# Optimization experiments

Measured on AMD Instinct MI355X. Metric: run time of the kernel, lower is better.

## Reference

```python
import jax, jax.numpy as jnp
import numpy as np

NEG_SLOPE = 0.2  # PyG GATConv LeakyReLU slope


def _gat_conv(x, ei, W, a_src, a_dst, bias, concat):
    # x: [N, F_in], ei: [2, E] (with self-loops), W: [F_in, H*C], a_*: [H, C]
    N = x.shape[0]
    H, C = a_src.shape
    xp = (x @ W).reshape(N, H, C)                       # [N, H, C]
    src, dst = ei[0], ei[1]
    s_score = jnp.einsum('nhc,hc->nh', xp, a_src)       # [N, H]
    d_score = jnp.einsum('nhc,hc->nh', xp, a_dst)       # [N, H]
    e = jax.nn.leaky_relu(s_score[src] + d_score[dst], negative_slope=NEG_SLOPE)  # [E, H]
    # segment softmax over incoming edges of each dst node
    m = jax.ops.segment_max(e, dst, num_segments=N)     # [N, H]
    ex = jnp.exp(e - m[dst])                            # [E, H]
    den = jax.ops.segment_sum(ex, dst, num_segments=N)  # [N, H]
    alpha = ex / den[dst]                               # [E, H]
    msg = alpha[:, :, None] * xp[src]                   # [E, H, C]
    out = jax.ops.segment_sum(msg, dst, num_segments=N) # [N, H, C]
    out = out.reshape(N, H * C) if concat else out.mean(axis=1)
    return out + bias


def _add_self_loops(edge_index, num_nodes):
    ar = jnp.arange(num_nodes, dtype=edge_index.dtype)
    return jnp.concatenate([edge_index, jnp.stack([ar, ar])], axis=1)


def setup_inputs() -> dict:
    key = jax.random.key(0)
    ks = jax.random.split(key, 16)
    N, E, F_in, Hd, heads, out_c, G = 50000, 800000, 128, 64, 4, 10, 64
    x = jax.random.normal(ks[0], (N, F_in), dtype=jnp.float32)
    edge_index = jax.random.randint(ks[1], (2, E), 0, N, dtype=jnp.int64)
    batch = jnp.sort(jax.random.randint(ks[2], (N,), 0, G, dtype=jnp.int64))
    sc = lambda f: 1.0 / np.sqrt(f)
    # layer 1: in -> hidden, heads=4, concat
    W1 = jax.random.normal(ks[3], (F_in, heads * Hd), dtype=jnp.float32) * sc(F_in)
    a_src1 = jax.random.normal(ks[4], (heads, Hd), dtype=jnp.float32) * sc(Hd)
    a_dst1 = jax.random.normal(ks[5], (heads, Hd), dtype=jnp.float32) * sc(Hd)
    b1 = jnp.zeros((heads * Hd,), dtype=jnp.float32)
    # layer 2: heads*hidden -> hidden, heads=1, concat=False
    W2 = jax.random.normal(ks[6], (heads * Hd, Hd), dtype=jnp.float32) * sc(heads * Hd)
    a_src2 = jax.random.normal(ks[7], (1, Hd), dtype=jnp.float32) * sc(Hd)
    a_dst2 = jax.random.normal(ks[8], (1, Hd), dtype=jnp.float32) * sc(Hd)
    b2 = jnp.zeros((Hd,), dtype=jnp.float32)
    # final linear
    Wl = jax.random.normal(ks[9], (Hd, out_c), dtype=jnp.float32) * sc(Hd)
    bl = jnp.zeros((out_c,), dtype=jnp.float32)
    return {"x": x, "edge_index": edge_index, "batch": batch,
            "W1": W1, "a_src1": a_src1, "a_dst1": a_dst1, "b1": b1,
            "W2": W2, "a_src2": a_src2, "a_dst2": a_dst2, "b2": b2,
            "Wl": Wl, "bl": bl}


def reference(x, edge_index, batch, W1, a_src1, a_dst1, b1,
              W2, a_src2, a_dst2, b2, Wl, bl):
    N = x.shape[0]
    G = 64  # number of graphs
    ei = _add_self_loops(edge_index, N)
    h = jax.nn.elu(_gat_conv(x, ei, W1, a_src1, a_dst1, b1, concat=True))
    h = jax.nn.elu(_gat_conv(h, ei, W2, a_src2, a_dst2, b2, concat=False))
    # global mean pool over graphs
    sums = jax.ops.segment_sum(h, batch, num_segments=G)            # [G, Hd]
    cnt = jax.ops.segment_sum(jnp.ones((N,), h.dtype), batch, num_segments=G)
    pooled = sums / jnp.maximum(cnt, 1.0)[:, None]
    return pooled @ Wl + bl
```

## Files before the change

kernel.cpp:

```cpp
#include <hip/hip_runtime.h>
#include <hip/hip_bf16.h>
#include <cstdint>

#define NN   50000
#define NE   800000
#define NET  850000
#define FIN  128
#define FH1  256
#define HD   64
#define NG   64
#define OUTC 10
#define NBS  ((NN + 255) / 256)

typedef __attribute__((ext_vector_type(8))) short short8v;
typedef __attribute__((ext_vector_type(4))) float f32x4;

__device__ __forceinline__ float bf2f(unsigned short u) {
    union { unsigned int i; float f; } v; v.i = ((unsigned int)u) << 16; return v.f;
}
__device__ __forceinline__ float bflo(unsigned int u) {
    union { unsigned int i; float f; } v; v.i = u << 16; return v.f;
}
__device__ __forceinline__ float bfhi(unsigned int u) {
    union { unsigned int i; float f; } v; v.i = u & 0xFFFF0000u; return v.f;
}
__device__ __forceinline__ unsigned short f2bf(float f) {
    union { float fl; unsigned int i; } v; v.fl = f;
    unsigned int x = v.i;
    return (unsigned short)((x + 0x7FFFu + ((x >> 16) & 1u)) >> 16);
}
__device__ __forceinline__ float leakyr(float v) { return v > 0.f ? v : 0.2f * v; }
__device__ __forceinline__ float elu1(float v)  { return v > 0.f ? v : expm1f(v); }

__global__ __launch_bounds__(256) void k_gemm1(
    const float* __restrict__ x, const float* __restrict__ W1,
    const float* __restrict__ asrc, const float* __restrict__ adst,
    unsigned short* __restrict__ xp1, float* __restrict__ s1t, float* __restrict__ d1)
{
    __shared__ __align__(16) short Ash[64 * 40];
    __shared__ __align__(16) short Bsh[256 * 40];
    int row0 = blockIdx.x * 64;
    int tid  = threadIdx.x;
    int wv   = tid >> 6;
    int lane = tid & 63;
    int g    = lane >> 4;
    int c    = lane & 15;

    f32x4 acc[4][4];
    #pragma unroll
    for (int i = 0; i < 4; i++)
        #pragma unroll
        for (int j = 0; j < 4; j++) acc[i][j] = (f32x4){0.f, 0.f, 0.f, 0.f};

    int sr = tid >> 2;
    int sq = tid & 3;

    for (int k0 = 0; k0 < FIN; k0 += 32) {
        {
            int gr = row0 + sr;
            float4 v0 = make_float4(0,0,0,0), v1 = make_float4(0,0,0,0);
            if (gr < NN) {
                const float4* p = reinterpret_cast<const float4*>(x + (size_t)gr * FIN + k0 + sq * 8);
                v0 = p[0]; v1 = p[1];
            }
            short8v pk;
            pk[0] = (short)f2bf(v0.x); pk[1] = (short)f2bf(v0.y);
            pk[2] = (short)f2bf(v0.z); pk[3] = (short)f2bf(v0.w);
            pk[4] = (short)f2bf(v1.x); pk[5] = (short)f2bf(v1.y);
            pk[6] = (short)f2bf(v1.z); pk[7] = (short)f2bf(v1.w);
            *reinterpret_cast<short8v*>(&Ash[sr * 40 + sq * 8]) = pk;
        }
        {
            #pragma unroll
            for (int kg = 0; kg < 4; kg++) {
                short8v pk;
                #pragma unroll
                for (int i = 0; i < 8; i++)
                    pk[i] = (short)f2bf(W1[(size_t)(k0 + kg * 8 + i) * FH1 + tid]);
                *reinterpret_cast<short8v*>(&Bsh[tid * 40 + kg * 8]) = pk;
            }
        }
        __syncthreads();
        short8v bf[4];
        #pragma unroll
        for (int j = 0; j < 4; j++)
            bf[j] = *reinterpret_cast<const short8v*>(&Bsh[(64 * wv + 16 * j + c) * 40 + g * 8]);
        #pragma unroll
        for (int rt = 0; rt < 4; rt++) {
            short8v af = *reinterpret_cast<const short8v*>(&Ash[(16 * rt + c) * 40 + g * 8]);
            #pragma unroll
            for (int j = 0; j < 4; j++)
                acc[rt][j] = __builtin_amdgcn_mfma_f32_16x16x32_bf16(af, bf[j], acc[rt][j], 0, 0, 0);
        }
        __syncthreads();
    }

    int n0 = 64 * wv;
    float as[4], ad[4];
    #pragma unroll
    for (int j = 0; j < 4; j++) {
        as[j] = asrc[n0 + 16 * j + c];
        ad[j] = adst[n0 + 16 * j + c];
    }
    #pragma unroll
    for (int rt = 0; rt < 4; rt++) {
        #pragma unroll
        for (int r = 0; r < 4; r++) {
            int row = row0 + 16 * rt + 4 * g + r;
            float sv = 0.f, dv = 0.f;
            #pragma unroll
            for (int j = 0; j < 4; j++) {
                float v = acc[rt][j][r];
                sv = fmaf(v, as[j], sv);
                dv = fmaf(v, ad[j], dv);
                if (row < NN) xp1[(size_t)row * FH1 + n0 + 16 * j + c] = f2bf(v);
            }
            #pragma unroll
            for (int off = 8; off >= 1; off >>= 1) {
                sv += __shfl_xor(sv, off, 16);
                dv += __shfl_xor(dv, off, 16);
            }
            if (c == 0 && row < NN) {
                s1t[(size_t)wv * NN + row] = sv;
                d1[row * 4 + wv] = dv;
            }
        }
    }
}

__global__ __launch_bounds__(256) void k_hist(
    const int* __restrict__ ei, int* __restrict__ deg)
{
    int e = blockIdx.x * 256 + threadIdx.x;
    if (e >= NET) return;
    int dst = (e < NE) ? ei[NE + e] : (e - NE);
    atomicAdd(&deg[dst], 1);
}

__global__ __launch_bounds__(256) void k_scan_a(
    const int* __restrict__ deg, int* __restrict__ part)
{
    __shared__ int sm[256];
    int t = threadIdx.x;
    int idx = blockIdx.x * 256 + t;
    sm[t] = (idx < NN) ? deg[idx] : 0;
    __syncthreads();
    for (int off = 128; off >= 1; off >>= 1) {
        if (t < off) sm[t] += sm[t + off];
        __syncthreads();
    }
    if (t == 0) part[blockIdx.x] = sm[0];
}

__global__ __launch_bounds__(256) void k_scan_b(
    int* __restrict__ part, int* __restrict__ rowptr)
{
    __shared__ int sm[256];
    int t = threadIdx.x;
    int v = (t < NBS) ? part[t] : 0;
    sm[t] = v;
    __syncthreads();
    for (int off = 1; off < 256; off <<= 1) {
        int u = (t >= off) ? sm[t - off] : 0;
        __syncthreads();
        sm[t] += u;
        __syncthreads();
    }
    if (t < NBS) part[t] = sm[t] - v;
    if (t == 0) rowptr[NN] = NET;
}

__global__ __launch_bounds__(256) void k_scan_c(
    const int* __restrict__ deg, const int* __restrict__ part,
    int* __restrict__ rowptr)
{
    __shared__ int sm[256];
    int t = threadIdx.x;
    int idx = blockIdx.x * 256 + t;
    int v = (idx < NN) ? deg[idx] : 0;
    sm[t] = v;
    __syncthreads();
    for (int off = 1; off < 256; off <<= 1) {
        int u = (t >= off) ? sm[t - off] : 0;
        __syncthreads();
        sm[t] += u;
        __syncthreads();
    }
    if (idx < NN) rowptr[idx] = part[blockIdx.x] + sm[t] - v;
}

__global__ __launch_bounds__(256) void k_scatter(
    const int* __restrict__ ei, const int* __restrict__ rowptr,
    int* __restrict__ cursor, int* __restrict__ eidx)
{
    int e = blockIdx.x * 256 + threadIdx.x;
    if (e >= NET) return;
    int src, dst;
    if (e < NE) { src = ei[e]; dst = ei[NE + e]; }
    else        { src = dst = e - NE; }
    int pos = atomicAdd(&cursor[dst], 1);
    eidx[rowptr[dst] + pos] = src;
}

__global__ __launch_bounds__(256) void k_pull1(
    const int* __restrict__ rowptr, const int* __restrict__ eidx,
    const float* __restrict__ s1t, const float* __restrict__ d1,
    const unsigned short* __restrict__ xp1, const float* __restrict__ b1,
    unsigned short* __restrict__ h1)
{
    int wv = threadIdx.x >> 6;
    int lane = threadIdx.x & 63;
    int n = blockIdx.x * 4 + wv;
    if (n >= NN) return;
    int head = lane >> 4;
    int c0 = lane * 4;
    int hNN = head * NN;
    float dv = d1[(size_t)n * 4 + head];
    int jb = __builtin_amdgcn_readfirstlane(rowptr[n]);
    int je = __builtin_amdgcn_readfirstlane(rowptr[n + 1]);
    float a0 = 0.f, a1 = 0.f, a2 = 0.f, a3 = 0.f;
    float den = 0.f;
    int j = jb;
    for (; j + 8 <= je; j += 8) {
        int s[8];
        #pragma unroll
        for (int q = 0; q < 8; q++) s[q] = eidx[j + q];
        float sc[8];
        uint2 u[8];
        #pragma unroll
        for (int q = 0; q < 8; q++) {
            const float* srow = s1t + s[q];
            sc[q] = srow[hNN];
            const unsigned short* xrow = xp1 + (size_t)s[q] * FH1;
            u[q] = *reinterpret_cast<const uint2*>(xrow + c0);
        }
        #pragma unroll
        for (int q = 0; q < 8; q++) {
            float ex = __expf(leakyr(sc[q] + dv));
            a0 = fmaf(bflo(u[q].x), ex, a0);
            a1 = fmaf(bfhi(u[q].x), ex, a1);
            a2 = fmaf(bflo(u[q].y), ex, a2);
            a3 = fmaf(bfhi(u[q].y), ex, a3);
            den += ex;
        }
    }
    for (; j < je; j++) {
        int src = eidx[j];
        const float* srow = s1t + src;
        float ex = __expf(leakyr(srow[hNN] + dv));
        const unsigned short* xrow = xp1 + (size_t)src * FH1;
        uint2 u = *reinterpret_cast<const uint2*>(xrow + c0);
        a0 = fmaf(bflo(u.x), ex, a0);
        a1 = fmaf(bfhi(u.x), ex, a1);
        a2 = fmaf(bflo(u.y), ex, a2);
        a3 = fmaf(bfhi(u.y), ex, a3);
        den += ex;
    }
    float inv = 1.0f / den;
    float4 b = *reinterpret_cast<const float4*>(b1 + c0);
    ushort4 st;
    st.x = f2bf(elu1(fmaf(a0, inv, b.x)));
    st.y = f2bf(elu1(fmaf(a1, inv, b.y)));
    st.z = f2bf(elu1(fmaf(a2, inv, b.z)));
    st.w = f2bf(elu1(fmaf(a3, inv, b.w)));
    *reinterpret_cast<ushort4*>(h1 + (size_t)n * FH1 + c0) = st;
}

__global__ __launch_bounds__(256) void k_gemm2(
    const unsigned short* __restrict__ h1, const float* __restrict__ W2,
    const float* __restrict__ asrc2, const float* __restrict__ adst2,
    unsigned short* __restrict__ xp2, float* __restrict__ s2, float* __restrict__ d2)
{
    __shared__ __align__(16) short Ash[64 * 40];
    __shared__ __align__(16) short Bsh[64 * 40];
    int row0 = blockIdx.x * 64;
    int tid  = threadIdx.x;
    int wv   = tid >> 6;
    int lane = tid & 63;
    int g    = lane >> 4;
    int c    = lane & 15;

    f32x4 acc[4] = {{0,0,0,0},{0,0,0,0},{0,0,0,0},{0,0,0,0}};

    int sr = tid >> 2;
    int sq = tid & 3;

    for (int k0 = 0; k0 < FH1; k0 += 32) {
        {
            int gr = row0 + sr;
            uint4 v = make_uint4(0, 0, 0, 0);
            if (gr < NN) v = *reinterpret_cast<const uint4*>(h1 + (size_t)gr * FH1 + k0 + sq * 8);
            *reinterpret_cast<uint4*>(&Ash[sr * 40 + sq * 8]) = v;
        }
        {
            int n  = tid & 63;
            int kg = tid >> 6;
            short8v pk;
            #pragma unroll
            for (int i = 0; i < 8; i++)
                pk[i] = (short)f2bf(W2[(size_t)(k0 + kg * 8 + i) * HD + n]);
            *reinterpret_cast<short8v*>(&Bsh[n * 40 + kg * 8]) = pk;
        }
        __syncthreads();
        short8v af = *reinterpret_cast<const short8v*>(&Ash[(16 * wv + c) * 40 + g * 8]);
        #pragma unroll
        for (int j = 0; j < 4; j++) {
            short8v bf = *reinterpret_cast<const short8v*>(&Bsh[(16 * j + c) * 40 + g * 8]);
            acc[j] = __builtin_amdgcn_mfma_f32_16x16x32_bf16(af, bf, acc[j], 0, 0, 0);
        }
        __syncthreads();
    }

    float as[4], ad[4];
    #pragma unroll
    for (int j = 0; j < 4; j++) {
        as[j] = asrc2[16 * j + c];
        ad[j] = adst2[16 * j + c];
    }
    #pragma unroll
    for (int r = 0; r < 4; r++) {
        int row = row0 + 16 * wv + 4 * g + r;
        float sv = 0.f, dv = 0.f;
        #pragma unroll
        for (int j = 0; j < 4; j++) {
            float v = acc[j][r];
            sv = fmaf(v, as[j], sv);
            dv = fmaf(v, ad[j], dv);
            if (row < NN) xp2[(size_t)row * HD + 16 * j + c] = f2bf(v);
        }
        #pragma unroll
        for (int off = 8; off >= 1; off >>= 1) {
            sv += __shfl_xor(sv, off, 16);
            dv += __shfl_xor(dv, off, 16);
        }
        if (c == 0 && row < NN) { s2[row] = sv; d2[row] = dv; }
    }
}

__global__ __launch_bounds__(256) void k_pull2(
    const int* __restrict__ rowptr, const int* __restrict__ eidx,
    const float* __restrict__ s2, const float* __restrict__ d2,
    const unsigned short* __restrict__ xp2, const float* __restrict__ b2,
    float* __restrict__ h2)
{
    int wv = threadIdx.x >> 6;
    int lane = threadIdx.x & 63;
    int n = blockIdx.x * 4 + wv;
    if (n >= NN) return;
    int half = lane >> 5;
    int c = lane & 31;
    float dv = d2[n];
    int jb = __builtin_amdgcn_readfirstlane(rowptr[n]);
    int je = __builtin_amdgcn_readfirstlane(rowptr[n + 1]);
    float a0 = 0.f, a1 = 0.f, den = 0.f;
    int j = jb;
    for (; j + 16 <= je; j += 16) {
        #pragma unroll
        for (int p = 0; p < 8; p++) {
            int e = j + 2 * p + half;
            int src = eidx[e];
            float sc = s2[src];
            unsigned int u = *reinterpret_cast<const unsigned int*>(xp2 + (size_t)src * HD + 2 * c);
            float ex = __expf(leakyr(sc + dv));
            a0 = fmaf(bflo(u), ex, a0);
            a1 = fmaf(bfhi(u), ex, a1);
            den += ex;
        }
    }
    for (; j < je; j += 2) {
        int e = j + half;
        bool valid = e < je;
        int ec = valid ? e : (je - 1);
        int src = eidx[ec];
        float sc = s2[src];
        unsigned int u = *reinterpret_cast<const unsigned int*>(xp2 + (size_t)src * HD + 2 * c);
        float ex = valid ? __expf(leakyr(sc + dv)) : 0.f;
        a0 = fmaf(bflo(u), ex, a0);
        a1 = fmaf(bfhi(u), ex, a1);
        den += ex;
    }
    a0 += __shfl_xor(a0, 32);
    a1 += __shfl_xor(a1, 32);
    den += __shfl_xor(den, 32);
    if (half == 0) {
        float inv = 1.0f / den;
        float2 bb = *reinterpret_cast<const float2*>(b2 + 2 * c);
        float2 o;
        o.x = elu1(fmaf(a0, inv, bb.x));
        o.y = elu1(fmaf(a1, inv, bb.y));
        *reinterpret_cast<float2*>(h2 + (size_t)n * HD + 2 * c) = o;
    }
}

__global__ __launch_bounds__(256) void k_pool(
    const float* __restrict__ h2, const int* __restrict__ batch,
    float* __restrict__ pooled )
{
    int g = blockIdx.x;
    int sslice = blockIdx.y;
    int lo = 0, hi = NN;
    while (lo < hi) { int m = (lo + hi) >> 1; if (batch[m] < g) lo = m + 1; else hi = m; }
    int start = lo;
    hi = NN;
    while (lo < hi) { int m = (lo + hi) >> 1; if (batch[m] < g + 1) lo = m + 1; else hi = m; }
    int end = lo;
    int len = end - start;
    int chunk = (len + 7) >> 3;
    int b0 = start + sslice * chunk;
    int b1 = min(b0 + chunk, end);
    int c = threadIdx.x & 63;
    int rg = threadIdx.x >> 6;
    float sum = 0.f;
    for (int n = b0 + rg; n < b1; n += 4)
        sum += h2[(size_t)n * HD + c];
    __shared__ float red[4][64];
    red[rg][c] = sum;
    __syncthreads();
    if (threadIdx.x < 64) {
        float tot = red[0][c] + red[1][c] + red[2][c] + red[3][c];
        if (tot != 0.f) atomicAdd(&pooled[g * HD + c], tot);
    }
}

__global__ __launch_bounds__(256) void k_final(
    const float* __restrict__ pooled, const int* __restrict__ batch,
    const float* __restrict__ Wl, const float* __restrict__ bl,
    float* __restrict__ out)
{
    int t = blockIdx.x * 256 + threadIdx.x;
    if (t >= NG * OUTC) return;
    int g = t / OUTC, o = t % OUTC;
    int lo = 0, hi = NN;
    while (lo < hi) { int m = (lo + hi) >> 1; if (batch[m] < g) lo = m + 1; else hi = m; }
    int start = lo;
    hi = NN;
    while (lo < hi) { int m = (lo + hi) >> 1; if (batch[m] < g + 1) lo = m + 1; else hi = m; }
    float cnt = (float)(lo - start);
    float acc = 0.f;
    #pragma unroll
    for (int k = 0; k < HD; k++)
        acc = fmaf(pooled[g * HD + k], Wl[k * OUTC + o], acc);
    out[t] = acc / fmaxf(cnt, 1.f) + bl[o];
}

extern "C" void kernel_launch(void* const* d_in, const int* in_sizes, int n_in,
                              void* d_out, int out_size, void* d_ws, size_t ws_size,
                              hipStream_t stream) {
    const float* x     = (const float*)d_in[0];
    const int*   ei    = (const int*)d_in[1];
    const int*   batch = (const int*)d_in[2];
    const float* W1    = (const float*)d_in[3];
    const float* as1   = (const float*)d_in[4];
    const float* ad1   = (const float*)d_in[5];
    const float* b1    = (const float*)d_in[6];
    const float* W2    = (const float*)d_in[7];
    const float* as2   = (const float*)d_in[8];
    const float* ad2   = (const float*)d_in[9];
    const float* b2    = (const float*)d_in[10];
    const float* Wl    = (const float*)d_in[11];
    const float* bl    = (const float*)d_in[12];
    float* out = (float*)d_out;

    char* w = (char*)d_ws;
    size_t off = 0;
    auto alloc = [&](size_t bytes) {
        void* p = (void*)(w + off);
        off = (off + bytes + 255) & ~(size_t)255;
        return p;
    };
    int* deg    = (int*)alloc((size_t)NN * 4);
    int* cursor = (int*)alloc((size_t)NN * 4);
    float* pooled = (float*)alloc((size_t)NG * HD * 4);
    size_t zbytes = off;
    int* part   = (int*)alloc((size_t)NBS * 4);
    int* rowptr = (int*)alloc((size_t)(NN + 1) * 4);
    int* eidx   = (int*)alloc((size_t)NET * 4);
    unsigned short* xp1 = (unsigned short*)alloc((size_t)NN * FH1 * 2);
    unsigned short* h1  = (unsigned short*)alloc((size_t)NN * FH1 * 2);
    float* s1t = (float*)alloc((size_t)NN * 4 * 4);
    float* d1s = (float*)alloc((size_t)NN * 4 * 4);
    unsigned short* xp2 = (unsigned short*)alloc((size_t)NN * HD * 2);
    float* s2  = (float*)alloc((size_t)NN * 4);
    float* d2s = (float*)alloc((size_t)NN * 4);
    float* h2  = (float*)alloc((size_t)NN * HD * 4);

    hipMemsetAsync(d_ws, 0, zbytes, stream);

    k_hist   <<<(NET + 255) / 256, 256, 0, stream>>>(ei, deg);
    k_scan_a <<<NBS, 256, 0, stream>>>(deg, part);
    k_scan_b <<<1, 256, 0, stream>>>(part, rowptr);
    k_scan_c <<<NBS, 256, 0, stream>>>(deg, part, rowptr);
    k_scatter<<<(NET + 255) / 256, 256, 0, stream>>>(ei, rowptr, cursor, eidx);

    k_gemm1<<<(NN + 63) / 64, 256, 0, stream>>>(x, W1, as1, ad1, xp1, s1t, d1s);
    k_pull1<<<(NN + 3) / 4, 256, 0, stream>>>(rowptr, eidx, s1t, d1s, xp1, b1, h1);
    k_gemm2<<<(NN + 63) / 64, 256, 0, stream>>>(h1, W2, as2, ad2, xp2, s2, d2s);
    k_pull2<<<(NN + 3) / 4, 256, 0, stream>>>(rowptr, eidx, s2, d2s, xp2, b2, h2);
    dim3 gp(NG, 8);
    k_pool <<<gp, 256, 0, stream>>>(h2, batch, pooled);
    k_final<<<(NG * OUTC + 255) / 256, 256, 0, stream>>>(pooled, batch, Wl, bl, out);
}
```

Baseline: 257.2 us.

## Store layer-1 projections head-major and split pull1 aggregation per head

The GEMM1 output xp1 is stored head-major ([head][node][64]) instead of node-major with all heads interleaved. pull1 now launches one wave per (node, head) pair, with block indices swizzled so that neighbouring blocks share a head. Each lane gathers one bf16 element per edge from a smaller per-head table, and only one score is read per wave. The goal is better cache locality, since each head's table is a quarter of the full projection. The cost is four times as many edge-index reads and exp evaluations, plus narrower 2-byte gathers per lane.

```diff
diff --git a/kernel.cpp b/kernel.cpp
--- a/kernel.cpp
+++ b/kernel.cpp
@@ -95,12 +95,11 @@
         __syncthreads();
     }
 
-    int n0 = 64 * wv;
     float as[4], ad[4];
     #pragma unroll
     for (int j = 0; j < 4; j++) {
-        as[j] = asrc[n0 + 16 * j + c];
-        ad[j] = adst[n0 + 16 * j + c];
+        as[j] = asrc[64 * wv + 16 * j + c];
+        ad[j] = adst[64 * wv + 16 * j + c];
     }
     #pragma unroll
     for (int rt = 0; rt < 4; rt++) {
@@ -113,7 +112,7 @@
                 float v = acc[rt][j][r];
                 sv = fmaf(v, as[j], sv);
                 dv = fmaf(v, ad[j], dv);
-                if (row < NN) xp1[(size_t)row * FH1 + n0 + 16 * j + c] = f2bf(v);
+                if (row < NN) xp1[((size_t)wv * NN + row) * HD + 16 * j + c] = f2bf(v);
             }
             #pragma unroll
             for (int off = 8; off >= 1; off >>= 1) {
@@ -208,62 +207,46 @@
     const unsigned short* __restrict__ xp1, const float* __restrict__ b1,
     unsigned short* __restrict__ h1)
 {
+    int b = blockIdx.x;
+    int head = (b >> 1) & 3;
+    int ng = ((b >> 3) << 1) | (b & 1);
     int wv = threadIdx.x >> 6;
     int lane = threadIdx.x & 63;
-    int n = blockIdx.x * 4 + wv;
+    int n = ng * 4 + wv;
     if (n >= NN) return;
-    int head = lane >> 4;
-    int c0 = lane * 4;
-    int hNN = head * NN;
+    const float* sh = s1t + (size_t)head * NN;
+    const unsigned short* xph = xp1 + (size_t)head * NN * HD;
     float dv = d1[(size_t)n * 4 + head];
     int jb = __builtin_amdgcn_readfirstlane(rowptr[n]);
     int je = __builtin_amdgcn_readfirstlane(rowptr[n + 1]);
-    float a0 = 0.f, a1 = 0.f, a2 = 0.f, a3 = 0.f;
-    float den = 0.f;
+    float a = 0.f, den = 0.f;
     int j = jb;
     for (; j + 8 <= je; j += 8) {
         int s[8];
         #pragma unroll
         for (int q = 0; q < 8; q++) s[q] = eidx[j + q];
         float sc[8];
-        uint2 u[8];
+        unsigned short xv[8];
         #pragma unroll
         for (int q = 0; q < 8; q++) {
-            const float* srow = s1t + s[q];
-            sc[q] = srow[hNN];
-            const unsigned short* xrow = xp1 + (size_t)s[q] * FH1;
-            u[q] = *reinterpret_cast<const uint2*>(xrow + c0);
+            sc[q] = sh[s[q]];
+            xv[q] = xph[(size_t)s[q] * HD + lane];
         }
         #pragma unroll
         for (int q = 0; q < 8; q++) {
             float ex = __expf(leakyr(sc[q] + dv));
-            a0 = fmaf(bflo(u[q].x), ex, a0);
-            a1 = fmaf(bfhi(u[q].x), ex, a1);
-            a2 = fmaf(bflo(u[q].y), ex, a2);
-            a3 = fmaf(bfhi(u[q].y), ex, a3);
+            a = fmaf(bf2f(xv[q]), ex, a);
             den += ex;
         }
     }
     for (; j < je; j++) {
         int src = eidx[j];
-        const float* srow = s1t + src;
-        float ex = __expf(leakyr(srow[hNN] + dv));
-        const unsigned short* xrow = xp1 + (size_t)src * FH1;
-        uint2 u = *reinterpret_cast<const uint2*>(xrow + c0);
-        a0 = fmaf(bflo(u.x), ex, a0);
-        a1 = fmaf(bfhi(u.x), ex, a1);
-        a2 = fmaf(bflo(u.y), ex, a2);
-        a3 = fmaf(bfhi(u.y), ex, a3);
+        float ex = __expf(leakyr(sh[src] + dv));
+        a = fmaf(bf2f(xph[(size_t)src * HD + lane]), ex, a);
         den += ex;
     }
-    float inv = 1.0f / den;
-    float4 b = *reinterpret_cast<const float4*>(b1 + c0);
-    ushort4 st;
-    st.x = f2bf(elu1(fmaf(a0, inv, b.x)));
-    st.y = f2bf(elu1(fmaf(a1, inv, b.y)));
-    st.z = f2bf(elu1(fmaf(a2, inv, b.z)));
-    st.w = f2bf(elu1(fmaf(a3, inv, b.w)));
-    *reinterpret_cast<ushort4*>(h1 + (size_t)n * FH1 + c0) = st;
+    float o = elu1(a / den + b1[head * HD + lane]);
+    h1[(size_t)n * FH1 + head * HD + lane] = f2bf(o);
 }
 
 __global__ __launch_bounds__(256) void k_gemm2(
@@ -493,7 +476,7 @@
     k_scatter<<<(NET + 255) / 256, 256, 0, stream>>>(ei, rowptr, cursor, eidx);
 
     k_gemm1<<<(NN + 63) / 64, 256, 0, stream>>>(x, W1, as1, ad1, xp1, s1t, d1s);
-    k_pull1<<<(NN + 3) / 4, 256, 0, stream>>>(rowptr, eidx, s1t, d1s, xp1, b1, h1);
+    k_pull1<<<NN, 256, 0, stream>>>(rowptr, eidx, s1t, d1s, xp1, b1, h1);
     k_gemm2<<<(NN + 63) / 64, 256, 0, stream>>>(h1, W2, as2, ad2, xp2, s2, d2s);
     k_pull2<<<(NN + 3) / 4, 256, 0, stream>>>(rowptr, eidx, s2, d2s, xp2, b2, h2);
     dim3 gp(NG, 8);
```

Measured after the change: 309.7 us. +20.4%, slower.

## Precompute per-edge attention exponentials in CSR order before the pull kernels

Applied to the files above, without the earlier changes.

Layer-1 edge weights exp(leakyrelu(s+d)) for all four heads are now computed during the CSR scatter, which moves gemm1 ahead of the graph build. They are stored in CSR order so that pull1 reads them contiguously instead of doing a random gather from s1t per edge. A new edge kernel does the same for layer 2, using a stored dst array. This replaces random gathers and per-lane exps in the pull kernels with coalesced streams, at the cost of extra edge-sized buffers, more writes, and one additional launch.

```diff
diff --git a/kernel.cpp b/kernel.cpp
--- a/kernel.cpp
+++ b/kernel.cpp
@@ -35,7 +35,7 @@
 __global__ __launch_bounds__(256) void k_gemm1(
     const float* __restrict__ x, const float* __restrict__ W1,
     const float* __restrict__ asrc, const float* __restrict__ adst,
-    unsigned short* __restrict__ xp1, float* __restrict__ s1t, float* __restrict__ d1)
+    unsigned short* __restrict__ xp1, float* __restrict__ s1, float* __restrict__ d1)
 {
     __shared__ __align__(16) short Ash[64 * 40];
     __shared__ __align__(16) short Bsh[256 * 40];
@@ -121,7 +121,7 @@
                 dv += __shfl_xor(dv, off, 16);
             }
             if (c == 0 && row < NN) {
-                s1t[(size_t)wv * NN + row] = sv;
+                s1[row * 4 + wv] = sv;
                 d1[row * 4 + wv] = dv;
             }
         }
@@ -191,7 +191,9 @@
 
 __global__ __launch_bounds__(256) void k_scatter(
     const int* __restrict__ ei, const int* __restrict__ rowptr,
-    int* __restrict__ cursor, int* __restrict__ eidx)
+    int* __restrict__ cursor, int* __restrict__ eidx, int* __restrict__ dsta,
+    const float* __restrict__ s1, const float* __restrict__ d1,
+    float* __restrict__ es1)
 {
     int e = blockIdx.x * 256 + threadIdx.x;
     if (e >= NET) return;
@@ -199,12 +201,22 @@
     if (e < NE) { src = ei[e]; dst = ei[NE + e]; }
     else        { src = dst = e - NE; }
     int pos = atomicAdd(&cursor[dst], 1);
-    eidx[rowptr[dst] + pos] = src;
+    int p = rowptr[dst] + pos;
+    eidx[p] = src;
+    dsta[p] = dst;
+    float4 s = *reinterpret_cast<const float4*>(s1 + (size_t)src * 4);
+    float4 d = *reinterpret_cast<const float4*>(d1 + (size_t)dst * 4);
+    float4 es;
+    es.x = __expf(leakyr(s.x + d.x));
+    es.y = __expf(leakyr(s.y + d.y));
+    es.z = __expf(leakyr(s.z + d.z));
+    es.w = __expf(leakyr(s.w + d.w));
+    *reinterpret_cast<float4*>(es1 + (size_t)p * 4) = es;
 }
 
 __global__ __launch_bounds__(256) void k_pull1(
     const int* __restrict__ rowptr, const int* __restrict__ eidx,
-    const float* __restrict__ s1t, const float* __restrict__ d1,
+    const float* __restrict__ es1,
     const unsigned short* __restrict__ xp1, const float* __restrict__ b1,
     unsigned short* __restrict__ h1)
 {
@@ -214,8 +226,6 @@
     if (n >= NN) return;
     int head = lane >> 4;
     int c0 = lane * 4;
-    int hNN = head * NN;
-    float dv = d1[(size_t)n * 4 + head];
     int jb = __builtin_amdgcn_readfirstlane(rowptr[n]);
     int je = __builtin_amdgcn_readfirstlane(rowptr[n + 1]);
     float a0 = 0.f, a1 = 0.f, a2 = 0.f, a3 = 0.f;
@@ -225,18 +235,16 @@
         int s[8];
         #pragma unroll
         for (int q = 0; q < 8; q++) s[q] = eidx[j + q];
-        float sc[8];
+        float es[8];
         uint2 u[8];
         #pragma unroll
         for (int q = 0; q < 8; q++) {
-            const float* srow = s1t + s[q];
-            sc[q] = srow[hNN];
-            const unsigned short* xrow = xp1 + (size_t)s[q] * FH1;
-            u[q] = *reinterpret_cast<const uint2*>(xrow + c0);
+            es[q] = es1[(size_t)(j + q) * 4 + head];
+            u[q] = *reinterpret_cast<const uint2*>(xp1 + (size_t)s[q] * FH1 + c0);
         }
         #pragma unroll
         for (int q = 0; q < 8; q++) {
-            float ex = __expf(leakyr(sc[q] + dv));
+            float ex = es[q];
             a0 = fmaf(bflo(u[q].x), ex, a0);
             a1 = fmaf(bfhi(u[q].x), ex, a1);
             a2 = fmaf(bflo(u[q].y), ex, a2);
@@ -246,10 +254,8 @@
     }
     for (; j < je; j++) {
         int src = eidx[j];
-        const float* srow = s1t + src;
-        float ex = __expf(leakyr(srow[hNN] + dv));
-        const unsigned short* xrow = xp1 + (size_t)src * FH1;
-        uint2 u = *reinterpret_cast<const uint2*>(xrow + c0);
+        float ex = es1[(size_t)j * 4 + head];
+        uint2 u = *reinterpret_cast<const uint2*>(xp1 + (size_t)src * FH1 + c0);
         a0 = fmaf(bflo(u.x), ex, a0);
         a1 = fmaf(bfhi(u.x), ex, a1);
         a2 = fmaf(bflo(u.y), ex, a2);
@@ -337,9 +343,21 @@
     }
 }
 
+__global__ __launch_bounds__(256) void k_edge2(
+    const int* __restrict__ eidx, const int* __restrict__ dsta,
+    const float* __restrict__ s2, const float* __restrict__ d2,
+    float* __restrict__ es2)
+{
+    int j = blockIdx.x * 256 + threadIdx.x;
+    if (j >= NET) return;
+    int src = eidx[j];
+    int dst = dsta[j];
+    es2[j] = __expf(leakyr(s2[src] + d2[dst]));
+}
+
 __global__ __launch_bounds__(256) void k_pull2(
     const int* __restrict__ rowptr, const int* __restrict__ eidx,
-    const float* __restrict__ s2, const float* __restrict__ d2,
+    const float* __restrict__ es2,
     const unsigned short* __restrict__ xp2, const float* __restrict__ b2,
     float* __restrict__ h2)
 {
@@ -349,7 +367,6 @@
     if (n >= NN) return;
     int half = lane >> 5;
     int c = lane & 31;
-    float dv = d2[n];
     int jb = __builtin_amdgcn_readfirstlane(rowptr[n]);
     int je = __builtin_amdgcn_readfirstlane(rowptr[n + 1]);
     float a0 = 0.f, a1 = 0.f, den = 0.f;
@@ -359,9 +376,8 @@
         for (int p = 0; p < 8; p++) {
             int e = j + 2 * p + half;
             int src = eidx[e];
-            float sc = s2[src];
+            float ex = es2[e];
             unsigned int u = *reinterpret_cast<const unsigned int*>(xp2 + (size_t)src * HD + 2 * c);
-            float ex = __expf(leakyr(sc + dv));
             a0 = fmaf(bflo(u), ex, a0);
             a1 = fmaf(bfhi(u), ex, a1);
             den += ex;
@@ -372,9 +388,8 @@
         bool valid = e < je;
         int ec = valid ? e : (je - 1);
         int src = eidx[ec];
-        float sc = s2[src];
+        float ex = valid ? es2[ec] : 0.f;
         unsigned int u = *reinterpret_cast<const unsigned int*>(xp2 + (size_t)src * HD + 2 * c);
-        float ex = valid ? __expf(leakyr(sc + dv)) : 0.f;
         a0 = fmaf(bflo(u), ex, a0);
         a1 = fmaf(bfhi(u), ex, a1);
         den += ex;
@@ -475,9 +490,12 @@
     int* part   = (int*)alloc((size_t)NBS * 4);
     int* rowptr = (int*)alloc((size_t)(NN + 1) * 4);
     int* eidx   = (int*)alloc((size_t)NET * 4);
+    int* dsta   = (int*)alloc((size_t)NET * 4);
+    float* es1  = (float*)alloc((size_t)NET * 4 * 4);
+    float* es2  = (float*)alloc((size_t)NET * 4);
     unsigned short* xp1 = (unsigned short*)alloc((size_t)NN * FH1 * 2);
     unsigned short* h1  = (unsigned short*)alloc((size_t)NN * FH1 * 2);
-    float* s1t = (float*)alloc((size_t)NN * 4 * 4);
+    float* s1  = (float*)alloc((size_t)NN * 4 * 4);
     float* d1s = (float*)alloc((size_t)NN * 4 * 4);
     unsigned short* xp2 = (unsigned short*)alloc((size_t)NN * HD * 2);
     float* s2  = (float*)alloc((size_t)NN * 4);
@@ -486,16 +504,17 @@
 
     hipMemsetAsync(d_ws, 0, zbytes, stream);
 
+    k_gemm1<<<(NN + 63) / 64, 256, 0, stream>>>(x, W1, as1, ad1, xp1, s1, d1s);
     k_hist   <<<(NET + 255) / 256, 256, 0, stream>>>(ei, deg);
     k_scan_a <<<NBS, 256, 0, stream>>>(deg, part);
     k_scan_b <<<1, 256, 0, stream>>>(part, rowptr);
     k_scan_c <<<NBS, 256, 0, stream>>>(deg, part, rowptr);
-    k_scatter<<<(NET + 255) / 256, 256, 0, stream>>>(ei, rowptr, cursor, eidx);
-
-    k_gemm1<<<(NN + 63) / 64, 256, 0, stream>>>(x, W1, as1, ad1, xp1, s1t, d1s);
-    k_pull1<<<(NN + 3) / 4, 256, 0, stream>>>(rowptr, eidx, s1t, d1s, xp1, b1, h1);
+    k_scatter<<<(NET + 255) / 256, 256, 0, stream>>>(ei, rowptr, cursor, eidx, dsta, s1, d1s, es1);
+
+    k_pull1<<<(NN + 3) / 4, 256, 0, stream>>>(rowptr, eidx, es1, xp1, b1, h1);
     k_gemm2<<<(NN + 63) / 64, 256, 0, stream>>>(h1, W2, as2, ad2, xp2, s2, d2s);
-    k_pull2<<<(NN + 3) / 4, 256, 0, stream>>>(rowptr, eidx, s2, d2s, xp2, b2, h2);
+    k_edge2<<<(NET + 255) / 256, 256, 0, stream>>>(eidx, dsta, s2, d2s, es2);
+    k_pull2<<<(NN + 3) / 4, 256, 0, stream>>>(rowptr, eidx, es2, xp2, b2, h2);
     dim3 gp(NG, 8);
     k_pool <<<gp, 256, 0, stream>>>(h2, batch, pooled);
     k_final<<<(NG * OUTC + 255) / 256, 256, 0, stream>>>(pooled, batch, Wl, bl, out);
```

Measured after the change: 269.6 us. 1.05x slower.
